# Performance work log

Hardware: AMD Instinct MI355X
Metric: run time of the kernel (lower is better)

## Reference

```python
import jax, jax.numpy as jnp
import numpy as np

B, S, C = 32, 512, 384
MAX_LEN = 4096
MAX_DUR = 16


def setup_inputs() -> dict:
    key = jax.random.key(0)
    kx, kd = jax.random.split(key)
    x = jax.random.normal(kx, (B, S, C), dtype=jnp.float32)
    durations = jax.random.randint(kd, (B, S), 0, MAX_DUR, dtype=jnp.int32)
    return {"x": x, "durations": durations, "max_length": MAX_LEN}


def reference(x, durations, max_length):
    # Round (no-op for int durations, kept for faithfulness to torch.round().long())
    d = jnp.round(durations.astype(jnp.float32)).astype(jnp.int32)  # [B, S]
    # _limit_durations is equivalent to clipping the cumulative sum at max_length:
    # the first token crossing max_length gets truncated, all later tokens zeroed.
    ends = jnp.clip(jnp.cumsum(d, axis=1), 0, max_length)          # [B, S]
    total = ends[:, -1]                                            # [B]
    t = jnp.arange(max_length, dtype=jnp.int32)                    # [T]
    # frame t belongs to phoneme j where starts[j] <= t < ends[j];
    # searchsorted(ends, t, 'right') skips zero-duration tokens automatically.
    idx = jax.vmap(lambda e: jnp.searchsorted(e, t, side='right'))(ends)  # [B, T]
    mel_masks = t[None, :] >= total[:, None]                       # [B, T] True = pad
    idx_c = jnp.clip(idx, 0, x.shape[1] - 1)
    expanded = jnp.take_along_axis(x, idx_c[:, :, None], axis=1)   # [B, T, C]
    expanded = jnp.where(mel_masks[:, :, None], jnp.zeros((), x.dtype), expanded)
    return expanded, mel_masks
```

## Files before the change

kernel.cpp:

```cpp
#include <hip/hip_runtime.h>

#define BATCH 32
#define SEQ 512
#define CH4 96
#define MAXL 4096
#define ZBLK 64
#define FBLKS (BATCH * SEQ)
#define THREADS 128

typedef float v4f __attribute__((ext_vector_type(4)));
typedef int   v4i __attribute__((ext_vector_type(4)));

__global__ __launch_bounds__(THREADS) void lr_fused(
    const v4f* __restrict__ x,
    const v4i* __restrict__ dur4,
    const int* __restrict__ max_len_p,
    v4f* __restrict__ out,
    float* __restrict__ out_mask)
{
    __shared__ int s_end[SEQ];

    const int tid = threadIdx.x;
    const int bid = blockIdx.x;
    const bool is_frame = (bid < FBLKS);
    const int b = is_frame ? (bid >> 9) : ((bid - FBLKS) >> 6);

    if (tid < 64) {
        const v4i* dp = dur4 + b * (SEQ / 4) + tid * 2;
        v4i d0 = dp[0], d1 = dp[1];
        int lane_sum = d0.x + d0.y + d0.z + d0.w + d1.x + d1.y + d1.z + d1.w;
        int incl = lane_sum;
        #pragma unroll
        for (int off = 1; off < 64; off <<= 1) {
            int v = __shfl_up(incl, off, 64);
            if (tid >= off) incl += v;
        }
        int cum = incl - lane_sum;
        const int maxlen = max_len_p[0];
        const int base = tid * 8;
        cum += d0.x; s_end[base + 0] = min(cum, maxlen);
        cum += d0.y; s_end[base + 1] = min(cum, maxlen);
        cum += d0.z; s_end[base + 2] = min(cum, maxlen);
        cum += d0.w; s_end[base + 3] = min(cum, maxlen);
        cum += d1.x; s_end[base + 4] = min(cum, maxlen);
        cum += d1.y; s_end[base + 5] = min(cum, maxlen);
        cum += d1.z; s_end[base + 6] = min(cum, maxlen);
        cum += d1.w; s_end[base + 7] = min(cum, maxlen);
    }
    __syncthreads();

    if (is_frame) {
        const int j  = bid & (SEQ - 1);
        const int e  = s_end[j];
        const int st = j ? s_end[j - 1] : 0;
        const int n  = e - st;
        if (n <= 0) return;
        if (tid < n)
            out_mask[(b << 12) + st + tid] = 0.0f;
        if (tid < CH4) {
            v4f v = x[(size_t)bid * CH4 + tid];
            v4f* ob = out + ((size_t)(b << 12) + st) * CH4 + tid;
            for (int k = 0; k < n; ++k) {
                *ob = v;
                ob += CH4;
            }
        }
    } else {
        const int i = (bid - FBLKS) & (ZBLK - 1);
        const int total = s_end[SEQ - 1];
        const v4f zero = (v4f){0.f, 0.f, 0.f, 0.f};
        for (int t = total + i; t < MAXL; t += ZBLK) {
            if (tid < CH4)
                out[((size_t)(b << 12) + t) * CH4 + tid] = zero;
            else if (tid == CH4)
                out_mask[(b << 12) + t] = 1.0f;
        }
    }
}

extern "C" void kernel_launch(void* const* d_in, const int* in_sizes, int n_in,
                              void* d_out, int out_size, void* d_ws, size_t ws_size,
                              hipStream_t stream) {
    const v4f* x = (const v4f*)d_in[0];
    const v4i* dur4 = (const v4i*)d_in[1];
    const int* max_len_p = (const int*)d_in[2];
    float* out = (float*)d_out;
    float* out_mask = out + (size_t)BATCH * MAXL * CH4 * 4;

    lr_fused<<<FBLKS + BATCH * ZBLK, THREADS, 0, stream>>>(
        x, dur4, max_len_p, (v4f*)out, out_mask);
}
```

Measured before the change: 216.2 us.

## Process eight phonemes per block and merge zero-fill into the same blocks

Replaces the one-block-per-phoneme grid plus separate zero-fill blocks with 2048 uniform blocks. Each block handles 8 consecutive phonemes and a strided share of the padding frames. This cuts how often the per-batch duration prefix scan is recomputed, from once per phoneme to once per 8 phonemes. It also issues the x loads before the scan so they overlap it. The trade-off is less parallelism and more serial stores per thread, and the load balance across blocks now depends on the durations.

```diff
diff --git a/kernel.cpp b/kernel.cpp
--- a/kernel.cpp
+++ b/kernel.cpp
@@ -4,8 +4,8 @@
 #define SEQ 512
 #define CH4 96
 #define MAXL 4096
-#define ZBLK 64
-#define FBLKS (BATCH * SEQ)
+#define FPB 8
+#define CPB 64
 #define THREADS 128
 
 typedef float v4f __attribute__((ext_vector_type(4)));
@@ -20,10 +20,18 @@
 {
     __shared__ int s_end[SEQ];
 
-    const int tid = threadIdx.x;
-    const int bid = blockIdx.x;
-    const bool is_frame = (bid < FBLKS);
-    const int b = is_frame ? (bid >> 9) : ((bid - FBLKS) >> 6);
+    const int tid   = threadIdx.x;
+    const int bid   = blockIdx.x;
+    const int b     = bid >> 6;
+    const int chunk = bid & (CPB - 1);
+    const int j0    = chunk * FPB;
+
+    v4f vx[FPB];
+    if (tid < CH4) {
+        const v4f* xp = x + ((size_t)(b * SEQ + j0)) * CH4 + tid;
+        #pragma unroll
+        for (int fr = 0; fr < FPB; ++fr) vx[fr] = xp[fr * CH4];
+    }
 
     if (tid < 64) {
         const v4i* dp = dur4 + b * (SEQ / 4) + tid * 2;
@@ -49,32 +57,34 @@
     }
     __syncthreads();
 
-    if (is_frame) {
-        const int j  = bid & (SEQ - 1);
-        const int e  = s_end[j];
-        const int st = j ? s_end[j - 1] : 0;
-        const int n  = e - st;
-        if (n <= 0) return;
-        if (tid < n)
-            out_mask[(b << 12) + st + tid] = 0.0f;
-        if (tid < CH4) {
-            v4f v = x[(size_t)bid * CH4 + tid];
-            v4f* ob = out + ((size_t)(b << 12) + st) * CH4 + tid;
-            for (int k = 0; k < n; ++k) {
+    const int st0   = j0 ? s_end[j0 - 1] : 0;
+    const int e7    = s_end[j0 + FPB - 1];
+    const int total = s_end[SEQ - 1];
+
+    if (tid < e7 - st0) out_mask[(b << 12) + st0 + tid] = 0.0f;
+
+    if (tid < CH4) {
+        v4f* const ob_base = out + ((size_t)(b << 12)) * CH4 + tid;
+        #pragma unroll
+        for (int fr = 0; fr < FPB; ++fr) {
+            const int jj = j0 + fr;
+            const int e  = s_end[jj];
+            const int st = jj ? s_end[jj - 1] : 0;
+            v4f v = vx[fr];
+            v4f* ob = ob_base + (size_t)st * CH4;
+            for (int t = st; t < e; ++t) {
                 *ob = v;
                 ob += CH4;
             }
         }
-    } else {
-        const int i = (bid - FBLKS) & (ZBLK - 1);
-        const int total = s_end[SEQ - 1];
-        const v4f zero = (v4f){0.f, 0.f, 0.f, 0.f};
-        for (int t = total + i; t < MAXL; t += ZBLK) {
-            if (tid < CH4)
-                out[((size_t)(b << 12) + t) * CH4 + tid] = zero;
-            else if (tid == CH4)
-                out_mask[(b << 12) + t] = 1.0f;
-        }
+    }
+
+    const v4f zero = (v4f){0.f, 0.f, 0.f, 0.f};
+    for (int t = total + chunk; t < MAXL; t += CPB) {
+        if (tid < CH4)
+            out[((size_t)(b << 12) + t) * CH4 + tid] = zero;
+        else if (tid == CH4)
+            out_mask[(b << 12) + t] = 1.0f;
     }
 }
 
@@ -87,6 +97,6 @@
     float* out = (float*)d_out;
     float* out_mask = out + (size_t)BATCH * MAXL * CH4 * 4;
 
-    lr_fused<<<FBLKS + BATCH * ZBLK, THREADS, 0, stream>>>(
+    lr_fused<<<BATCH * CPB, THREADS, 0, stream>>>(
         x, dur4, max_len_p, (v4f*)out, out_mask);
 }
```

New measurement: 215.1 us. No clear change (-0.5%).
